# Optimization experiments

Measured on AMD Instinct MI355X. Metric: run time of the kernel, lower is better.

## Reference

```python
import jax, jax.numpy as jnp
import numpy as np

B, N, L = 1, 128, 256
D_MSA, D_HID, D_PAIR = 256, 32, 128
EPS = 1e-5


def setup_inputs() -> dict:
    key = jax.random.key(0)
    ks = jax.random.split(key, 8)
    msa = jax.random.normal(ks[0], (B, N, L, D_MSA), dtype=jnp.float32)
    pair = jax.random.normal(ks[1], (B, L, L, D_PAIR), dtype=jnp.float32)
    symmids = jax.random.randint(ks[2], (1,), 0, 1, dtype=jnp.int64)
    symmsub = jax.random.randint(ks[3], (1,), 0, 1, dtype=jnp.int64)
    # learned params (lecun-normal-ish scale = 1/sqrt(fan_in))
    ln_gamma = jnp.ones((D_MSA,), jnp.float32)
    ln_beta = jnp.zeros((D_MSA,), jnp.float32)
    w_left = jax.random.normal(ks[4], (D_MSA, D_HID), jnp.float32) / np.sqrt(D_MSA)
    b_left = jnp.zeros((D_HID,), jnp.float32)
    w_right = jax.random.normal(ks[5], (D_MSA, D_HID), jnp.float32) / np.sqrt(D_MSA)
    b_right = jnp.zeros((D_HID,), jnp.float32)
    w_out = jax.random.normal(ks[6], (D_HID * D_HID, D_PAIR), jnp.float32) / np.sqrt(D_HID * D_HID)
    b_out = jnp.zeros((D_PAIR,), jnp.float32)
    return {
        "msa": msa, "pair": pair, "symmids": symmids, "symmsub": symmsub,
        "ln_gamma": ln_gamma, "ln_beta": ln_beta,
        "w_left": w_left, "b_left": b_left,
        "w_right": w_right, "b_right": b_right,
        "w_out": w_out, "b_out": b_out,
    }


def reference(msa, pair, symmids, symmsub, ln_gamma, ln_beta,
              w_left, b_left, w_right, b_right, w_out, b_out):
    b, n, l, _ = msa.shape
    # LayerNorm over d_msa (biased variance, matching torch)
    mu = jnp.mean(msa, axis=-1, keepdims=True)
    var = jnp.mean(jnp.square(msa - mu), axis=-1, keepdims=True)
    x = (msa - mu) * jax.lax.rsqrt(var + EPS) * ln_gamma + ln_beta
    left = x @ w_left + b_left                       # [b, n, l, d_h]
    right = (x @ w_right + b_right) / float(n)       # [b, n, l, d_h]
    # outer product, reduced over MSA (s) dim -> [b, l, m, d_h, d_h]
    out = jnp.einsum('bsli,bsmj->blmij', left, right).reshape(b, l, l, -1)
    out = out @ w_out + b_out                        # [b, l, l, d_pair]
    return pair + out
```

## Files before the change

### kernel.cpp

```cpp
#include <hip/hip_runtime.h>


typedef float v4f __attribute__((ext_vector_type(4)));
typedef short v8s __attribute__((ext_vector_type(8)));

static __device__ inline unsigned short f2bf(float x) {
    unsigned int u = __builtin_bit_cast(unsigned int, x);
    return (unsigned short)((u + 0x7fffu + ((u >> 16) & 1u)) >> 16);
}

__global__ __launch_bounds__(256) void k_prep(const float* __restrict__ w_out,
                                              const float* __restrict__ wl,
                                              const float* __restrict__ wr,
                                              unsigned short* __restrict__ w2,
                                              unsigned short* __restrict__ wTg) {
    const int b = blockIdx.x, t = threadIdx.x;
    unsigned short tmp[8];
    if (b < 64) {
        int tgt = b * 2048 + t * 8;
        int p = (tgt >> 6) & 127;
        int ck = tgt >> 13, kc0 = tgt & 63;
        for (int e = 0; e < 8; ++e) {
            int kp = ck * 64 + kc0 + e;
            int j1 = (kp >> 9) & 1, qd = (kp >> 7) & 3, lp = (kp >> 3) & 15;
            int i1 = (kp >> 2) & 1, r = kp & 3;
            int ii = i1 * 16 + qd * 4 + r, jj = j1 * 16 + lp;
            tmp[e] = f2bf(w_out[(ii * 32 + jj) * 128 + p]);
        }
        *(uint4*)&w2[tgt] = *(const uint4*)tmp;
    } else {
        int tgt = (b - 64) * 2048 + t * 8;
        int c = tgt >> 8, d0 = tgt & 255;
        const float* src = (c < 32) ? wl : wr;
        int cc = c & 31;
        for (int e = 0; e < 8; ++e) tmp[e] = f2bf(src[(d0 + e) * 32 + cc]);
        *(uint4*)&wTg[tgt] = *(const uint4*)tmp;
    }
}

__global__ __launch_bounds__(256) void k_lnproj(
    const float* __restrict__ msa, const float* __restrict__ gamma, const float* __restrict__ beta,
    const unsigned short* __restrict__ wTg, const float* __restrict__ bl, const float* __restrict__ br,
    unsigned short* __restrict__ leftT, unsigned short* __restrict__ rightT) {
    __shared__ unsigned short xb[32 * 264];
    __shared__ unsigned short wlds[64 * 264];
    __shared__ unsigned short outT[64 * 40];

    const int t = threadIdx.x, lane = t & 63, w = t >> 6;
    const int l = blockIdx.x, s0 = blockIdx.y * 32;
    const int quad = lane >> 4, l15 = lane & 15;

    for (int it = 0; it < 8; ++it) {
        int idx = it * 2048 + t * 8;
        *(uint4*)&wlds[(idx >> 8) * 264 + (idx & 255)] = *(const uint4*)&wTg[idx];
    }

    float4 g4 = *(const float4*)&gamma[lane * 4];
    float4 be4 = *(const float4*)&beta[lane * 4];
    float4 vr[8]; float s1[8], s2[8];
    for (int r = 0; r < 8; ++r) {
        const float* row = msa + (size_t)((s0 + w * 8 + r) * 256 + l) * 256;
        vr[r] = *(const float4*)&row[lane * 4];
    }
    for (int r = 0; r < 8; ++r) {
        float4 v = vr[r];
        s1[r] = v.x + v.y + v.z + v.w;
        s2[r] = v.x * v.x + v.y * v.y + v.z * v.z + v.w * v.w;
    }
    for (int o = 32; o > 0; o >>= 1)
        for (int r = 0; r < 8; ++r) { s1[r] += __shfl_xor(s1[r], o); s2[r] += __shfl_xor(s2[r], o); }
    for (int r = 0; r < 8; ++r) {
        float mu = s1[r] * (1.f / 256);
        float rs = rsqrtf(s2[r] * (1.f / 256) - mu * mu + 1e-5f);
        float4 v = vr[r];
        ushort4 xs;
        xs.x = f2bf((v.x - mu) * rs * g4.x + be4.x);
        xs.y = f2bf((v.y - mu) * rs * g4.y + be4.y);
        xs.z = f2bf((v.z - mu) * rs * g4.z + be4.z);
        xs.w = f2bf((v.w - mu) * rs * g4.w + be4.w);
        *(ushort4*)&xb[(w * 8 + r) * 264 + lane * 4] = xs;
    }
    __syncthreads();

    const int mt = w >> 1, ntb = (w & 1) * 2;
    v4f acc[2] = {};
    const int frow = (mt * 16 + l15) * 264;
    for (int ks = 0; ks < 8; ++ks) {
        int k = ks * 32 + quad * 8;
        v8s a = *(const v8s*)&xb[frow + k];
        v8s b0 = *(const v8s*)&wlds[(ntb * 16 + l15) * 264 + k];
        v8s b1 = *(const v8s*)&wlds[((ntb + 1) * 16 + l15) * 264 + k];
        acc[0] = __builtin_amdgcn_mfma_f32_16x16x32_bf16(a, b0, acc[0], 0, 0, 0);
        acc[1] = __builtin_amdgcn_mfma_f32_16x16x32_bf16(a, b1, acc[1], 0, 0, 0);
    }

    for (int tn = 0; tn < 2; ++tn) {
        int c = (ntb + tn) * 16 + l15;
        float bias = c < 32 ? bl[c] : br[c - 32];
        float scale = c < 32 ? 1.f : (1.f / 128);
        for (int r = 0; r < 4; ++r)
            outT[c * 40 + mt * 16 + quad * 4 + r] = f2bf((acc[tn][r] + bias) * scale);
    }
    __syncthreads();

    {
        int c = t >> 2, q = t & 3;
        uint4 vv = *(const uint4*)&outT[c * 40 + q * 8];
        int kh = s0 >> 6;
        int g = ((s0 & 32) >> 3) + q;
        int g2 = g ^ (c & 7);
        unsigned short* dst = (c < 32) ? (leftT + l * 4096 + c * 128)
                                       : (rightT + l * 4096 + (c - 32) * 128);
        *(uint4*)&dst[kh * 64 + g2 * 8] = vv;
    }
}

__global__ __launch_bounds__(256) void k_outer(
    const unsigned short* __restrict__ leftT, const unsigned short* __restrict__ rightT,
    const unsigned short* __restrict__ w2g, const float* __restrict__ bout,
    const float* __restrict__ pairIn, float* __restrict__ out) {
    __shared__ alignas(16) unsigned short smem[24576];
    unsigned short* Ah = smem;
    unsigned short* Bh = smem + 8192;
    unsigned short* Obuf = smem;
    unsigned short* wbuf = smem + 16384;

    const int t = threadIdx.x, lane = t & 63, w = t >> 6;
    const int l0 = blockIdx.x * 4, m0 = blockIdx.y * 4;
    const int wm = w & 1, wn = w >> 1;
    const int quad = lane >> 4, l15 = lane & 15;

    const unsigned short* Asrc = leftT + l0 * 4096;
    const unsigned short* Bsrc = rightT + m0 * 4096;

    v4f acc[4][4] = {};
    for (int kh = 0; kh < 2; ++kh) {
        __syncthreads();
        for (int it = 0; it < 4; ++it) {
            int el = (it * 256 + t) * 8;
            int m = el >> 6, off = el & 63;
            *(uint4*)&Ah[m * 64 + off] = *(const uint4*)&Asrc[m * 128 + kh * 64 + off];
            *(uint4*)&Bh[m * 64 + off] = *(const uint4*)&Bsrc[m * 128 + kh * 64 + off];
        }
        __syncthreads();
        for (int ks = 0; ks < 2; ++ks) {
            int g = ks * 4 + quad;
            v8s a[4], bb[4];
            for (int i = 0; i < 4; ++i)
                a[i] = *(const v8s*)&Ah[(wm * 64 + i * 16 + l15) * 64 + ((g ^ (l15 & 7)) << 3)];
            for (int j = 0; j < 4; ++j)
                bb[j] = *(const v8s*)&Bh[(wn * 64 + j * 16 + l15) * 64 + ((g ^ (l15 & 7)) << 3)];
            for (int i = 0; i < 4; ++i)
                for (int j = 0; j < 4; ++j)
                    acc[i][j] = __builtin_amdgcn_mfma_f32_16x16x32_bf16(a[i], bb[j], acc[i][j], 0, 0, 0);
        }
    }
    __syncthreads();

    for (int a2 = 0; a2 < 2; ++a2)
        for (int b2 = 0; b2 < 2; ++b2) {
            int pr = (wm * 2 + a2) * 4 + wn * 2 + b2;
            for (int j1 = 0; j1 < 2; ++j1) {
                unsigned short tmp8[8];
                for (int i1 = 0; i1 < 2; ++i1)
                    for (int r = 0; r < 4; ++r)
                        tmp8[i1 * 4 + r] = f2bf(acc[a2 * 2 + i1][b2 * 2 + j1][r]);
                int pg = (j1 * 64 + lane) ^ (pr & 7);
                *(uint4*)&Obuf[pr * 1024 + pg * 8] = *(const uint4*)tmp8;
            }
        }
    __syncthreads();

    v4f acc2[2] = {};
    {
        const unsigned short* wsrc = w2g + w * 2048;
        unsigned short* wb = wbuf + w * 2048;
        int wa[4];
        uint4 pf[4];
        for (int u = 0; u < 4; ++u) {
            int g2 = (lane & 1) * 4 + u;
            wa[u] = (lane >> 1) * 64 + ((g2 ^ ((lane >> 1) & 7)) << 3);
            pf[u] = *(const uint4*)&wsrc[lane * 32 + u * 8];
        }
        for (int ck = 0; ck < 16; ++ck) {
            for (int u = 0; u < 4; ++u) *(uint4*)&wb[wa[u]] = pf[u];
            if (ck < 15)
                for (int u = 0; u < 4; ++u)
                    pf[u] = *(const uint4*)&wsrc[(ck + 1) * 8192 + lane * 32 + u * 8];
            for (int inner = 0; inner < 2; ++inner) {
                int g = ck * 8 + inner * 4 + quad;
                v8s a = *(const v8s*)&Obuf[l15 * 1024 + ((g ^ (l15 & 7)) << 3)];
                for (int tt = 0; tt < 2; ++tt) {
                    v8s bfr = *(const v8s*)&wb[(tt * 16 + l15) * 64 + (((inner * 4 + quad) ^ (l15 & 7)) << 3)];
                    acc2[tt] = __builtin_amdgcn_mfma_f32_16x16x32_bf16(a, bfr, acc2[tt], 0, 0, 0);
                }
            }
        }
    }

    for (int tt = 0; tt < 2; ++tt) {
        int p = (w * 2 + tt) * 16 + l15;
        float bo = bout[p];
        for (int r = 0; r < 4; ++r) {
            int pr = quad * 4 + r;
            int dl = pr >> 2, dm = pr & 3;
            size_t idx = (size_t)((l0 + dl) * 256 + (m0 + dm)) * 128 + p;
            out[idx] = pairIn[idx] + bo + acc2[tt][r];
        }
    }
}

extern "C" void kernel_launch(void* const* d_in, const int* in_sizes, int n_in,
                              void* d_out, int out_size, void* d_ws, size_t ws_size,
                              hipStream_t stream) {
    const float* msa   = (const float*)d_in[0];
    const float* pairI = (const float*)d_in[1];
    const float* gamma = (const float*)d_in[4];
    const float* beta  = (const float*)d_in[5];
    const float* wl    = (const float*)d_in[6];
    const float* bl    = (const float*)d_in[7];
    const float* wr    = (const float*)d_in[8];
    const float* br    = (const float*)d_in[9];
    const float* wout  = (const float*)d_in[10];
    const float* bout  = (const float*)d_in[11];
    float* out = (float*)d_out;

    unsigned short* leftT  = (unsigned short*)d_ws;
    unsigned short* rightT = leftT + 256 * 32 * 128;
    unsigned short* w2     = rightT + 256 * 32 * 128;
    unsigned short* wTg    = w2 + 131072;

    k_prep<<<dim3(72), 256, 0, stream>>>(wout, wl, wr, w2, wTg);
    k_lnproj<<<dim3(256, 4), 256, 0, stream>>>(msa, gamma, beta, wTg, bl, br, leftT, rightT);
    k_outer<<<dim3(64, 64), 256, 0, stream>>>(leftT, rightT, w2, bout, pairI, out);
}
```

Baseline: 200.4 us.

## Pre-swizzle w_out into MFMA fragment order and load it straight to registers

The prep kernel now writes w_out in the exact per-lane MFMA B-fragment order, so k_outer loads weight fragments directly from global memory into registers instead of staging them through LDS. This drops the 16KB weight buffer, shrinking shared memory from 48KB to 32KB. It also adds a launch-bounds occupancy hint of 4 blocks and an extra XOR swizzle bit on the Obuf layout to cut bank conflicts. In exchange, every wave issues its own global loads for the weights, relying on the L2 cache for reuse, and register pressure rises under the occupancy cap.

```diff
diff --git a/kernel.cpp b/kernel.cpp
--- a/kernel.cpp
+++ b/kernel.cpp
@@ -12,22 +12,24 @@
 __global__ __launch_bounds__(256) void k_prep(const float* __restrict__ w_out,
                                               const float* __restrict__ wl,
                                               const float* __restrict__ wr,
-                                              unsigned short* __restrict__ w2,
+                                              unsigned short* __restrict__ w3,
                                               unsigned short* __restrict__ wTg) {
     const int b = blockIdx.x, t = threadIdx.x;
     unsigned short tmp[8];
     if (b < 64) {
         int tgt = b * 2048 + t * 8;
-        int p = (tgt >> 6) & 127;
-        int ck = tgt >> 13, kc0 = tgt & 63;
+        int lane6 = (tgt >> 3) & 63, quad = lane6 >> 4, l15 = lane6 & 15;
+        int w = (tgt >> 9) & 3, tt = (tgt >> 11) & 1;
+        int inner = (tgt >> 12) & 1, ck = tgt >> 13;
+        int p = w * 32 + tt * 16 + l15;
         for (int e = 0; e < 8; ++e) {
-            int kp = ck * 64 + kc0 + e;
+            int kp = ck * 64 + inner * 32 + quad * 8 + e;
             int j1 = (kp >> 9) & 1, qd = (kp >> 7) & 3, lp = (kp >> 3) & 15;
             int i1 = (kp >> 2) & 1, r = kp & 3;
             int ii = i1 * 16 + qd * 4 + r, jj = j1 * 16 + lp;
             tmp[e] = f2bf(w_out[(ii * 32 + jj) * 128 + p]);
         }
-        *(uint4*)&w2[tgt] = *(const uint4*)tmp;
+        *(uint4*)&w3[tgt] = *(const uint4*)tmp;
     } else {
         int tgt = (b - 64) * 2048 + t * 8;
         int c = tgt >> 8, d0 = tgt & 255;
@@ -115,15 +117,14 @@
     }
 }
 
-__global__ __launch_bounds__(256) void k_outer(
+__global__ __launch_bounds__(256, 4) void k_outer(
     const unsigned short* __restrict__ leftT, const unsigned short* __restrict__ rightT,
     const unsigned short* __restrict__ w2g, const float* __restrict__ bout,
     const float* __restrict__ pairIn, float* __restrict__ out) {
-    __shared__ alignas(16) unsigned short smem[24576];
+    __shared__ alignas(16) unsigned short smem[16384];
     unsigned short* Ah = smem;
     unsigned short* Bh = smem + 8192;
     unsigned short* Obuf = smem;
-    unsigned short* wbuf = smem + 16384;
 
     const int t = threadIdx.x, lane = t & 63, w = t >> 6;
     const int l0 = blockIdx.x * 4, m0 = blockIdx.y * 4;
@@ -139,8 +140,8 @@
         for (int it = 0; it < 4; ++it) {
             int el = (it * 256 + t) * 8;
             int m = el >> 6, off = el & 63;
-            *(uint4*)&Ah[m * 64 + off] = *(const uint4*)&Asrc[m * 128 + kh * 64 + off];
-            *(uint4*)&Bh[m * 64 + off] = *(const uint4*)&Bsrc[m * 128 + kh * 64 + off];
+            *(uint4*)&Ah[el] = *(const uint4*)&Asrc[m * 128 + kh * 64 + off];
+            *(uint4*)&Bh[el] = *(const uint4*)&Bsrc[m * 128 + kh * 64 + off];
         }
         __syncthreads();
         for (int ks = 0; ks < 2; ++ks) {
@@ -165,7 +166,7 @@
                 for (int i1 = 0; i1 < 2; ++i1)
                     for (int r = 0; r < 4; ++r)
                         tmp8[i1 * 4 + r] = f2bf(acc[a2 * 2 + i1][b2 * 2 + j1][r]);
-                int pg = (j1 * 64 + lane) ^ (pr & 7);
+                int pg = (j1 * 64 + lane) ^ (pr & 7) ^ ((pr & 8) << 3);
                 *(uint4*)&Obuf[pr * 1024 + pg * 8] = *(const uint4*)tmp8;
             }
         }
@@ -173,27 +174,32 @@
 
     v4f acc2[2] = {};
     {
-        const unsigned short* wsrc = w2g + w * 2048;
-        unsigned short* wb = wbuf + w * 2048;
-        int wa[4];
-        uint4 pf[4];
-        for (int u = 0; u < 4; ++u) {
-            int g2 = (lane & 1) * 4 + u;
-            wa[u] = (lane >> 1) * 64 + ((g2 ^ ((lane >> 1) & 7)) << 3);
-            pf[u] = *(const uint4*)&wsrc[lane * 32 + u * 8];
-        }
+        const unsigned short* wsrc = w2g + w * 512 + lane * 8;
+        v8s f0 = *(const v8s*)&wsrc[0];
+        v8s f1 = *(const v8s*)&wsrc[2048];
+        v8s f2 = *(const v8s*)&wsrc[4096];
+        v8s f3 = *(const v8s*)&wsrc[6144];
+#pragma unroll
         for (int ck = 0; ck < 16; ++ck) {
-            for (int u = 0; u < 4; ++u) *(uint4*)&wb[wa[u]] = pf[u];
-            if (ck < 15)
-                for (int u = 0; u < 4; ++u)
-                    pf[u] = *(const uint4*)&wsrc[(ck + 1) * 8192 + lane * 32 + u * 8];
-            for (int inner = 0; inner < 2; ++inner) {
-                int g = ck * 8 + inner * 4 + quad;
-                v8s a = *(const v8s*)&Obuf[l15 * 1024 + ((g ^ (l15 & 7)) << 3)];
-                for (int tt = 0; tt < 2; ++tt) {
-                    v8s bfr = *(const v8s*)&wb[(tt * 16 + l15) * 64 + (((inner * 4 + quad) ^ (l15 & 7)) << 3)];
-                    acc2[tt] = __builtin_amdgcn_mfma_f32_16x16x32_bf16(a, bfr, acc2[tt], 0, 0, 0);
-                }
+            v8s c0 = f0, c1 = f1, c2 = f2, c3 = f3;
+            if (ck < 15) {
+                const unsigned short* nx = wsrc + (ck + 1) * 8192;
+                f0 = *(const v8s*)&nx[0];
+                f1 = *(const v8s*)&nx[2048];
+                f2 = *(const v8s*)&nx[4096];
+                f3 = *(const v8s*)&nx[6144];
+            }
+            {
+                int g = ck * 8 + quad;
+                v8s a = *(const v8s*)&Obuf[l15 * 1024 + ((g ^ (l15 & 7) ^ ((l15 & 8) << 3)) << 3)];
+                acc2[0] = __builtin_amdgcn_mfma_f32_16x16x32_bf16(a, c0, acc2[0], 0, 0, 0);
+                acc2[1] = __builtin_amdgcn_mfma_f32_16x16x32_bf16(a, c1, acc2[1], 0, 0, 0);
+            }
+            {
+                int g = ck * 8 + 4 + quad;
+                v8s a = *(const v8s*)&Obuf[l15 * 1024 + ((g ^ (l15 & 7) ^ ((l15 & 8) << 3)) << 3)];
+                acc2[0] = __builtin_amdgcn_mfma_f32_16x16x32_bf16(a, c2, acc2[0], 0, 0, 0);
+                acc2[1] = __builtin_amdgcn_mfma_f32_16x16x32_bf16(a, c3, acc2[1], 0, 0, 0);
             }
         }
     }
@@ -227,10 +233,10 @@
 
     unsigned short* leftT  = (unsigned short*)d_ws;
     unsigned short* rightT = leftT + 256 * 32 * 128;
-    unsigned short* w2     = rightT + 256 * 32 * 128;
-    unsigned short* wTg    = w2 + 131072;
-
-    k_prep<<<dim3(72), 256, 0, stream>>>(wout, wl, wr, w2, wTg);
+    unsigned short* w3     = rightT + 256 * 32 * 128;
+    unsigned short* wTg    = w3 + 131072;
+
+    k_prep<<<dim3(72), 256, 0, stream>>>(wout, wl, wr, w3, wTg);
     k_lnproj<<<dim3(256, 4), 256, 0, stream>>>(msa, gamma, beta, wTg, bl, br, leftT, rightT);
-    k_outer<<<dim3(64, 64), 256, 0, stream>>>(leftT, rightT, w2, bout, pairI, out);
-}
+    k_outer<<<dim3(64, 64), 256, 0, stream>>>(leftT, rightT, w3, bout, pairI, out);
+}
```

Result: faster. 181.7 us (-9.3%).
